# Optimization experiments

Hardware: AMD Instinct MI355X
Metric: run time of the kernel (lower is better)

## Reference

```python
import jax, jax.numpy as jnp
import numpy as np

N = 512      # nodes
E = 512      # edges = nb-graph nodes
M = 16384    # nb-graph edges
FIN = 64     # in_node_nf
HID = 128    # hidden_nf
D = 32       # VTV_coord_nf (positional-encoding width)


def _silu(v):
    return v * jax.nn.sigmoid(v)


def _mlp(v, w1, b1, w2, b2):
    # 2-layer MLP with SiLU (matches MLP(in, out, [hidden]))
    return _silu(v @ w1 + b1) @ w2 + b2


def setup_inputs() -> dict:
    key = jax.random.key(0)
    ks = jax.random.split(key, 32)

    def lin(k, i, o, scale=None):
        s = (1.0 / np.sqrt(i)) if scale is None else scale
        return jax.random.normal(k, (i, o), dtype=jnp.float32) * jnp.float32(s)

    inp = {}
    inp['h'] = jax.random.normal(ks[0], (N, FIN), dtype=jnp.float32)
    inp['x'] = jax.random.normal(ks[1], (N, 3), dtype=jnp.float32)
    inp['edges'] = jax.random.randint(ks[2], (2, E), 0, N)
    inp['nb_edge'] = jax.random.randint(ks[3], (2, M), 0, E)
    inp['edge_attr'] = jax.random.normal(ks[4], (E, 4), dtype=jnp.float32)
    inp['nb_num_nodes'] = E  # python int (static)
    # edge_encoder: MLP(2*FIN -> HID -> FIN)
    inp['ew1'] = lin(ks[5], 2 * FIN, HID); inp['eb1'] = jnp.zeros((HID,), jnp.float32)
    inp['ew2'] = lin(ks[6], HID, FIN);     inp['eb2'] = jnp.zeros((FIN,), jnp.float32)
    # PPGN mlp1 / mlp2: MLP(D+FIN -> HID -> FIN)
    inp['p1w1'] = lin(ks[7], D + FIN, HID); inp['p1b1'] = jnp.zeros((HID,), jnp.float32)
    inp['p1w2'] = lin(ks[8], HID, FIN);     inp['p1b2'] = jnp.zeros((FIN,), jnp.float32)
    inp['p2w1'] = lin(ks[9], D + FIN, HID); inp['p2b1'] = jnp.zeros((HID,), jnp.float32)
    inp['p2w2'] = lin(ks[10], HID, FIN);    inp['p2b2'] = jnp.zeros((FIN,), jnp.float32)
    # PPGN output mlp: MLP(D+FIN+FIN -> HID -> FIN) on concat(skip, matmul)
    inp['p3w1'] = lin(ks[11], D + 2 * FIN, HID); inp['p3b1'] = jnp.zeros((HID,), jnp.float32)
    inp['p3w2'] = lin(ks[12], HID, FIN);         inp['p3b2'] = jnp.zeros((FIN,), jnp.float32)
    # IGN 2->1: linear over 5 basis ops
    inp['ign_w'] = lin(ks[13], 5 * FIN, FIN); inp['ign_b'] = jnp.zeros((FIN,), jnp.float32)
    # coord_mlp: Linear(FIN,HID), SiLU, Linear(HID,1,bias=False) with tiny init
    inp['cw1'] = lin(ks[14], FIN, HID); inp['cb1'] = jnp.zeros((HID,), jnp.float32)
    inp['cw2'] = lin(ks[15], HID, 1, scale=0.001)
    # node_dec: MLP(FIN -> HID -> FIN)
    inp['ndw1'] = lin(ks[16], FIN, HID); inp['ndb1'] = jnp.zeros((HID,), jnp.float32)
    inp['ndw2'] = lin(ks[17], HID, FIN); inp['ndb2'] = jnp.zeros((FIN,), jnp.float32)
    return inp


def reference(h, x, edges, nb_edge, edge_attr, nb_num_nodes,
              ew1, eb1, ew2, eb2,
              p1w1, p1b1, p1w2, p1b2,
              p2w1, p2b1, p2w2, p2b2,
              p3w1, p3b1, p3w2, p3b2,
              ign_w, ign_b,
              cw1, cb1, cw2,
              ndw1, ndb1, ndw2, ndb2):
    rows, cols = edges[0], edges[1]
    coord_diff = x[rows] - x[cols]                      # [E,3]
    nbr, nbc = nb_edge[0], nb_edge[1]
    # VTV: inner product of the two relative-position vectors of paired edges
    vtv = jnp.sum(coord_diff[nbr] * coord_diff[nbc], axis=-1)   # [M]
    # sinusoidal positional encoding, a_scale = D/2
    half = D // 2
    div_term = jnp.exp(jnp.log(jnp.float32(10000.0)) * (2.0 * jnp.arange(half, dtype=jnp.float32) / D))
    ang = vtv[:, None] * jnp.float32(D / 2) / div_term          # [M, D/2]
    pe = jnp.stack([jnp.sin(ang), jnp.cos(ang)], axis=-1).reshape(vtv.shape[0], D)
    # node-pair features per original edge
    efn = _mlp(jnp.concatenate([h[rows], h[cols]], axis=1), ew1, eb1, ew2, eb2)  # [E,FIN]
    nb_feat = jnp.concatenate([pe, efn[nbr] * efn[nbc]], axis=1)                 # [M, D+FIN]
    # densify nb-graph 2-tensor and run PPGN block
    En = nb_num_nodes
    T = jnp.zeros((En, En, nb_feat.shape[1]), dtype=nb_feat.dtype).at[nbr, nbc].add(nb_feat)
    m1 = _mlp(T, p1w1, p1b1, p1w2, p1b2)                 # [En,En,FIN]
    m2 = _mlp(T, p2w1, p2b1, p2w2, p2b2)
    mult = jnp.einsum('ikf,kjf->ijf', m1, m2)            # feature-wise matmul
    Tout = _mlp(jnp.concatenate([T, mult], axis=-1), p3w1, p3b1, p3w2, p3b2)
    # IGN 2->1: diag, row-sum, col-sum, total-sum, trace (broadcast)
    idx = jnp.arange(En)
    diag = Tout[idx, idx]                                # [En,FIN]
    rowsum = Tout.sum(axis=1)
    colsum = Tout.sum(axis=0)
    tot = jnp.broadcast_to(Tout.sum(axis=(0, 1)), diag.shape)
    tr = jnp.broadcast_to(diag.sum(axis=0), diag.shape)
    nb_t1 = jnp.concatenate([diag, rowsum, colsum, tot, tr], axis=1) @ ign_w + ign_b  # [En,FIN]
    # coord update: weighted coord_diff, segment-mean over source node
    w = _silu(nb_t1 @ cw1 + cb1) @ cw2                   # [E,1]
    trans = coord_diff * w
    Nn = x.shape[0]
    seg = jax.ops.segment_sum(trans, rows, num_segments=Nn)
    cnt = jax.ops.segment_sum(jnp.ones((rows.shape[0], 1), trans.dtype), rows, num_segments=Nn)
    x_new = x + seg / jnp.clip(cnt, 1.0)
    # node update: scatter_add edge features then residual MLP
    nb_t0 = jax.ops.segment_sum(nb_t1, rows, num_segments=Nn)
    h_new = h + _mlp(nb_t0, ndw1, ndb1, ndw2, ndb2)
    return (h_new, x_new, edge_attr)
```

## Files before the change

### kernel.cpp

```cpp
#include <hip/hip_runtime.h>
#include <hip/hip_bf16.h>

#define NN   512
#define EE   512
#define MM   16384

typedef float v4f __attribute__((ext_vector_type(4)));
typedef short short8v __attribute__((ext_vector_type(8)));

__device__ __forceinline__ float silu_f(float v) { return v / (1.0f + __expf(-v)); }

__global__ __launch_bounds__(128) void k_edge(
    const float* __restrict__ h, const float* __restrict__ x,
    const int* __restrict__ edges,
    const float* __restrict__ ew1, const float* __restrict__ eb1,
    const float* __restrict__ ew2, const float* __restrict__ eb2,
    float* __restrict__ coord_diff, float* __restrict__ efn) {
  __shared__ float hin[128];
  __shared__ float hs[128];
  int e = blockIdx.x;
  int t = threadIdx.x;
  int r = edges[e], c = edges[EE + e];
  if (t < 3) coord_diff[e * 3 + t] = x[r * 3 + t] - x[c * 3 + t];
  if (t < 64) { hin[t] = h[r * 64 + t]; hin[64 + t] = h[c * 64 + t]; }
  __syncthreads();
  float acc = eb1[t];
  for (int k = 0; k < 128; ++k) acc += hin[k] * ew1[k * 128 + t];
  hs[t] = silu_f(acc);
  __syncthreads();
  if (t < 64) {
    float o = eb2[t];
    for (int k = 0; k < 128; ++k) o += hs[k] * ew2[k * 64 + t];
    efn[e * 64 + t] = o;
  }
}

__global__ __launch_bounds__(128) void k_consts(
    const float* __restrict__ p1b1, const float* __restrict__ p1w2, const float* __restrict__ p1b2,
    const float* __restrict__ p2b1, const float* __restrict__ p2w2, const float* __restrict__ p2b2,
    float* __restrict__ c1, float* __restrict__ c2) {
  __shared__ float h1[128], h2[128];
  int t = threadIdx.x;
  h1[t] = silu_f(p1b1[t]); h2[t] = silu_f(p2b1[t]);
  __syncthreads();
  if (t < 64) {
    float a1 = p1b2[t], a2 = p2b2[t];
    for (int k = 0; k < 128; ++k) { a1 += h1[k] * p1w2[k * 64 + t]; a2 += h2[k] * p2w2[k * 64 + t]; }
    c1[t] = a1; c2[t] = a2;
  }
}

__global__ __launch_bounds__(256) void k_prep(const float* __restrict__ p3w1,
                                              __hip_bfloat16* __restrict__ Wt) {
  int e = blockIdx.x * 256 + threadIdx.x;
  int hh = e >> 6, f = e & 63;
  Wt[hh * 64 + f] = __float2bfloat16(p3w1[(96 + f) * 128 + hh]);
}

__global__ __launch_bounds__(256) void k_mark(const int* __restrict__ nb_edge,
                                              int* __restrict__ slotmap) {
  int m = blockIdx.x * 256 + threadIdx.x;
  if (m >= MM) return;
  int cell = nb_edge[m] * 512 + nb_edge[MM + m];
  atomicCAS(&slotmap[cell], -1, -2);
}

__global__ __launch_bounds__(256) void k_compact(int* __restrict__ slotmap,
                                                 int* __restrict__ slotmapT,
                                                 int* __restrict__ cells,
                                                 int* __restrict__ nC) {
  int cell = blockIdx.x * 256 + threadIdx.x;
  if (slotmap[cell] != -2) return;
  int s = atomicAdd(nC, 1);
  slotmap[cell] = s;
  slotmapT[(cell & 511) * 512 + (cell >> 9)] = s;
  cells[s] = cell;
}

__global__ __launch_bounds__(192) void k_scatterT(
    const int* __restrict__ nb_edge, const int* __restrict__ slotmap,
    const float* __restrict__ coord_diff, const float* __restrict__ efn,
    float* __restrict__ Tc) {
  int t = threadIdx.x;
  int sub = (t >= 96) ? 1 : 0;
  int c = t - sub * 96;
  int m = blockIdx.x * 2 + sub;
  int a = nb_edge[m], b = nb_edge[MM + m];
  int s = slotmap[a * 512 + b];
  float val;
  if (c < 32) {
    float vtv = coord_diff[a * 3 + 0] * coord_diff[b * 3 + 0]
              + coord_diff[a * 3 + 1] * coord_diff[b * 3 + 1]
              + coord_diff[a * 3 + 2] * coord_diff[b * 3 + 2];
    int i = c >> 1;
    float ang = vtv * 16.0f * __expf(-0.57564627324851143f * (float)i);
    val = (c & 1) ? cosf(ang) : sinf(ang);
  } else {
    int f = c - 32;
    val = efn[a * 64 + f] * efn[b * 64 + f];
  }
  atomicAdd(&Tc[s * 96 + c], val);
}

__global__ __launch_bounds__(128) void k_mlp96b(
    const int* __restrict__ cells, const int* __restrict__ nC, const float* __restrict__ Tc,
    const float* __restrict__ w11, const float* __restrict__ b11,
    const float* __restrict__ w12, const float* __restrict__ b12,
    const float* __restrict__ w21, const float* __restrict__ b21,
    const float* __restrict__ w22, const float* __restrict__ b22,
    const float* __restrict__ c1, const float* __restrict__ c2,
    const float* __restrict__ p3w1,
    float* __restrict__ D1, float* __restrict__ D2,
    float* __restrict__ A, float* __restrict__ B,
    float* __restrict__ TWc) {
  __shared__ float xsT[96 * 8];
  __shared__ float hid[8][128];
  __shared__ int cl[8];
  int t = threadIdx.x;
  int nc = *nC;
  int s0 = blockIdx.x * 8;
  if (s0 >= nc) return;
  for (int e = t; e < 768; e += 128) xsT[(e % 96) * 8 + e / 96] = Tc[s0 * 96 + e];
  if (t < 8) cl[t] = (s0 + t < nc) ? cells[s0 + t] : 0;
  __syncthreads();
  float tw[8], a1[8], a2[8];
#pragma unroll
  for (int c = 0; c < 8; ++c) { tw[c] = 0.f; a1[c] = b11[t]; a2[c] = b21[t]; }
  for (int k = 0; k < 96; ++k) {
    float wt = p3w1[k * 128 + t];
    float w1v = w11[k * 128 + t];
    float w2v = w21[k * 128 + t];
    float4 xlo = *(const float4*)&xsT[k * 8];
    float4 xhi = *(const float4*)&xsT[k * 8 + 4];
    float xv[8] = {xlo.x, xlo.y, xlo.z, xlo.w, xhi.x, xhi.y, xhi.z, xhi.w};
#pragma unroll
    for (int c = 0; c < 8; ++c) {
      tw[c] += xv[c] * wt; a1[c] += xv[c] * w1v; a2[c] += xv[c] * w2v;
    }
  }
#pragma unroll
  for (int c = 0; c < 8; ++c) {
    if (s0 + c < nc) TWc[(s0 + c) * 128 + t] = tw[c];
    hid[c][t] = silu_f(a1[c]);
  }
  __syncthreads();
  {
    int hh = t & 63, cq = t >> 6;
    float o[4];
#pragma unroll
    for (int cc = 0; cc < 4; ++cc) o[cc] = b12[hh];
    for (int k = 0; k < 128; ++k) {
      float w = w12[k * 64 + hh];
#pragma unroll
      for (int cc = 0; cc < 4; ++cc) o[cc] += hid[cq * 4 + cc][k] * w;
    }
#pragma unroll
    for (int cc = 0; cc < 4; ++cc) {
      int c = cq * 4 + cc;
      if (s0 + c < nc) {
        float d = o[cc] - c1[hh];
        D1[(s0 + c) * 64 + hh] = d;
        atomicAdd(&A[(cl[c] >> 9) * 64 + hh], d);
      }
    }
  }
  __syncthreads();
#pragma unroll
  for (int c = 0; c < 8; ++c) hid[c][t] = silu_f(a2[c]);
  __syncthreads();
  {
    int hh = t & 63, cq = t >> 6;
    float o[4];
#pragma unroll
    for (int cc = 0; cc < 4; ++cc) o[cc] = b22[hh];
    for (int k = 0; k < 128; ++k) {
      float w = w22[k * 64 + hh];
#pragma unroll
      for (int cc = 0; cc < 4; ++cc) o[cc] += hid[cq * 4 + cc][k] * w;
    }
#pragma unroll
    for (int cc = 0; cc < 4; ++cc) {
      int c = cq * 4 + cc;
      if (s0 + c < nc) {
        float d = o[cc] - c2[hh];
        D2[(s0 + c) * 64 + hh] = d;
        atomicAdd(&B[(cl[c] & 511) * 64 + hh], d);
      }
    }
  }
}

__global__ __launch_bounds__(128) void k_uv(
    const float* __restrict__ A, const float* __restrict__ B,
    const float* __restrict__ c1, const float* __restrict__ c2,
    const float* __restrict__ p3w1, const float* __restrict__ p3b1,
    float* __restrict__ u, float* __restrict__ v) {
  __shared__ float vec[64];
  int i = blockIdx.x, y = blockIdx.y, t = threadIdx.x;
  if (t < 64)
    vec[t] = (y == 0) ? (512.0f * c1[t] * c2[t] + c2[t] * A[i * 64 + t])
                      : (c1[t] * B[i * 64 + t]);
  __syncthreads();
  float a = (y == 0) ? p3b1[t] : 0.f;
  for (int f = 0; f < 64; ++f) a += vec[f] * p3w1[(96 + f) * 128 + t];
  (y == 0 ? u : v)[i * 128 + t] = a;
}

__global__ __launch_bounds__(512) void k_densify(
    const int* __restrict__ slotmap, const int* __restrict__ slotmapT,
    const float* __restrict__ D1, const float* __restrict__ D2,
    __hip_bfloat16* __restrict__ D1d, __hip_bfloat16* __restrict__ D2dT) {
  int k = threadIdx.x;
  int i = blockIdx.x;
  int y = blockIdx.y;
  if (y < 64) {
    int f = y;
    int s = slotmap[i * 512 + k];
    float v = (s >= 0) ? D1[s * 64 + f] : 0.f;
    D1d[(f * 512 + i) * 512 + k] = __float2bfloat16(v);
  } else {
    int f = y - 64;
    int s = slotmapT[i * 512 + k];
    float v = (s >= 0) ? D2[s * 64 + f] : 0.f;
    D2dT[(f * 512 + i) * 512 + k] = __float2bfloat16(v);
  }
}

__global__ __launch_bounds__(256) void k_einsum_mfma(
    const __hip_bfloat16* __restrict__ D1d,
    const __hip_bfloat16* __restrict__ D2dT,
    __hip_bfloat16* __restrict__ S_fij) {
  __shared__ short As[128 * 40];
  __shared__ short Bs[128 * 40];
  int b = blockIdx.x;
  int f = b >> 4;
  int i0 = ((b >> 2) & 3) * 128, j0 = (b & 3) * 128;
  int t = threadIdx.x;
  int w = t >> 6, lane = t & 63;
  int wy = w >> 1, wx = w & 1;
  int q = lane >> 4, l15 = lane & 15;
  const short* Ap = (const short*)D1d + f * 262144;
  const short* Bp = (const short*)D2dT + f * 262144;
  int row = t >> 1, seg = t & 1;
  v4f acc[4][4];
#pragma unroll
  for (int yi = 0; yi < 4; ++yi)
#pragma unroll
    for (int xj = 0; xj < 4; ++xj) acc[yi][xj] = (v4f){0.f, 0.f, 0.f, 0.f};
  for (int k0 = 0; k0 < 512; k0 += 32) {
    __syncthreads();
    const short8v* ga = (const short8v*)&Ap[(i0 + row) * 512 + k0 + seg * 16];
    const short8v* gb = (const short8v*)&Bp[(j0 + row) * 512 + k0 + seg * 16];
    *(short8v*)&As[row * 40 + seg * 16] = ga[0];
    *(short8v*)&As[row * 40 + seg * 16 + 8] = ga[1];
    *(short8v*)&Bs[row * 40 + seg * 16] = gb[0];
    *(short8v*)&Bs[row * 40 + seg * 16 + 8] = gb[1];
    __syncthreads();
    short8v af[4], bf[4];
#pragma unroll
    for (int x = 0; x < 4; ++x) {
      af[x] = *(const short8v*)&As[(wy * 64 + x * 16 + l15) * 40 + q * 8];
      bf[x] = *(const short8v*)&Bs[(wx * 64 + x * 16 + l15) * 40 + q * 8];
    }
#pragma unroll
    for (int yi = 0; yi < 4; ++yi)
#pragma unroll
      for (int xj = 0; xj < 4; ++xj)
        acc[yi][xj] = __builtin_amdgcn_mfma_f32_16x16x32_bf16(af[yi], bf[xj], acc[yi][xj], 0, 0, 0);
  }
#pragma unroll
  for (int yi = 0; yi < 4; ++yi)
#pragma unroll
    for (int r = 0; r < 4; ++r) {
      int irow = i0 + wy * 64 + yi * 16 + q * 4 + r;
#pragma unroll
      for (int xj = 0; xj < 4; ++xj)
        S_fij[(f * 512 + irow) * 512 + j0 + wx * 64 + xj * 16 + l15] =
            __float2bfloat16(acc[yi][xj][r]);
    }
}

__global__ __launch_bounds__(256) void k_transpose(
    const __hip_bfloat16* __restrict__ S_fij, __hip_bfloat16* __restrict__ S) {
  __shared__ short lds[64 * 72];
  int t = threadIdx.x;
  int ij0 = blockIdx.x * 64;
  const short* src = (const short*)S_fij;
#pragma unroll
  for (int p = 0; p < 2; ++p) {
    int f = p * 32 + (t >> 3), seg = t & 7;
    short8v ga = *(const short8v*)&src[f * 262144 + ij0 + seg * 8];
    int fgrp = f >> 3, flo = f & 7;
#pragma unroll
    for (int k = 0; k < 8; ++k) {
      int ij = seg * 8 + k;
      int swz = (fgrp ^ (ij & 7) ^ ((ij >> 3) & 7)) & 7;
      lds[ij * 72 + swz * 8 + flo] = ga[k];
    }
  }
  __syncthreads();
  short* dst = (short*)S;
#pragma unroll
  for (int p = 0; p < 2; ++p) {
    int ij = p * 32 + (t >> 3), fseg = t & 7;
    int swz = (fseg ^ (ij & 7) ^ ((ij >> 3) & 7)) & 7;
    short8v val = *(const short8v*)&lds[ij * 72 + swz * 8];
    *(short8v*)&dst[(ij0 + ij) * 64 + fseg * 8] = val;
  }
}

__global__ __launch_bounds__(256) void k_tout_mfma(
    const __hip_bfloat16* __restrict__ S, const float* __restrict__ u,
    const float* __restrict__ v, const float* __restrict__ TWc,
    const int* __restrict__ slotmap, const __hip_bfloat16* __restrict__ Wt,
    float* __restrict__ row_part, float* __restrict__ col_part,
    float* __restrict__ diag_silu) {
  __shared__ __hip_bfloat16 WtL[128 * 72];
  __shared__ float uvL[4096];
  __shared__ float colbuf[4][16][128];
  __shared__ int slotL[256];
  int t = threadIdx.x;
  int w = t >> 6, lane = t & 63;
  int q = lane >> 4, l15 = lane & 15;
  int bi = blockIdx.x >> 5, bj = blockIdx.x & 31;
  int i0 = bi * 16, j0 = bj * 16;
  for (int e = t; e < 4096; e += 256) {
    int row = e >> 5, c2 = e & 31;
    ((unsigned*)WtL)[row * 36 + c2] = ((const unsigned*)Wt)[row * 32 + c2];
  }
  for (int e = t; e < 2048; e += 256) uvL[e] = u[(i0 + (e >> 7)) * 128 + (e & 127)];
  for (int e = t; e < 2048; e += 256) uvL[2048 + e] = v[(j0 + (e >> 7)) * 128 + (e & 127)];
  slotL[t] = slotmap[(i0 + (t >> 4)) * 512 + j0 + (t & 15)];
  short8v a[4][2];
#pragma unroll
  for (int mt = 0; mt < 4; ++mt) {
    const short8v* sp =
        (const short8v*)&S[((i0 + w * 4 + mt) * 512 + j0 + l15) * 64];
    a[mt][0] = sp[q];
    a[mt][1] = sp[4 + q];
  }
  __syncthreads();
#pragma unroll
  for (int half = 0; half < 2; ++half) {
    v4f acc[4][4];
#pragma unroll
    for (int mt = 0; mt < 4; ++mt)
#pragma unroll
      for (int n4 = 0; n4 < 4; ++n4) {
        int nt = half * 4 + n4;
        const short8v* b0 = (const short8v*)&WtL[(nt * 16 + l15) * 72 + q * 8];
        const short8v* b1 = (const short8v*)&WtL[(nt * 16 + l15) * 72 + 32 + q * 8];
        v4f c = {0.f, 0.f, 0.f, 0.f};
        c = __builtin_amdgcn_mfma_f32_16x16x32_bf16(a[mt][0], *b0, c, 0, 0, 0);
        c = __builtin_amdgcn_mfma_f32_16x16x32_bf16(a[mt][1], *b1, c, 0, 0, 0);
        acc[mt][n4] = c;
      }
#pragma unroll
    for (int n4 = 0; n4 < 4; ++n4) {
      int nt = half * 4 + n4;
      int hh = nt * 16 + l15;
      float rs[4] = {0.f, 0.f, 0.f, 0.f};
#pragma unroll
      for (int r = 0; r < 4; ++r) {
        int jL = q * 4 + r;
        float cs = 0.f;
        float vv = uvL[2048 + jL * 128 + hh];
#pragma unroll
        for (int mt = 0; mt < 4; ++mt) {
          int iL = w * 4 + mt;
          float z = acc[mt][n4][r] + uvL[iL * 128 + hh] + vv;
          int s = slotL[iL * 16 + jL];
          if (s >= 0) z += TWc[s * 128 + hh];
          float sv = silu_f(z);
          rs[mt] += sv;
          cs += sv;
          if (bi == bj && iL == jL) diag_silu[(i0 + iL) * 128 + hh] = sv;
        }
        colbuf[w][jL][hh] = cs;
      }
#pragma unroll
      for (int mt = 0; mt < 4; ++mt) {
        float rsum = rs[mt];
        rsum += __shfl_xor(rsum, 16);
        rsum += __shfl_xor(rsum, 32);
        if (q == 0)
          row_part[(bj * 512 + i0 + w * 4 + mt) * 128 + hh] = rsum;
      }
    }
  }
  __syncthreads();
  for (int e = t; e < 2048; e += 256) {
    int jL = e >> 7, hh = e & 127;
    float acc4 = colbuf[0][jL][hh] + colbuf[1][jL][hh] +
                 colbuf[2][jL][hh] + colbuf[3][jL][hh];
    col_part[(bi * 512 + j0 + jL) * 128 + hh] = acc4;
  }
}

__global__ __launch_bounds__(256) void k_sumparts(
    const float* __restrict__ row_part, const float* __restrict__ col_part,
    float* __restrict__ rowsum, float* __restrict__ colsum) {
  int i = blockIdx.x, t = threadIdx.x;
  const float* src = (t < 128) ? row_part : col_part;
  float* dst = (t < 128) ? rowsum : colsum;
  int hc = t & 127;
  float a = 0.f;
  for (int p = 0; p < 32; ++p) a += src[(p * 512 + i) * 128 + hc];
  dst[i * 128 + hc] = a;
}

__global__ __launch_bounds__(64) void k_tout2(
    const float* __restrict__ diag_silu, const float* __restrict__ rowsum_silu,
    const float* __restrict__ colsum_silu,
    const float* __restrict__ w2, const float* __restrict__ b2,
    float* __restrict__ diag_T, float* __restrict__ row_T, float* __restrict__ col_T) {
  __shared__ float in[128];
  int e = blockIdx.x, which = blockIdx.y, t = threadIdx.x;
  const float* src = (which == 0) ? diag_silu : (which == 1) ? rowsum_silu : colsum_silu;
  in[t] = src[e * 128 + t]; in[64 + t] = src[e * 128 + 64 + t];
  __syncthreads();
  float a = 0.f;
  for (int k = 0; k < 128; ++k) a += in[k] * w2[k * 64 + t];
  float bias = b2[t] * ((which == 0) ? 1.0f : 512.0f);
  float* dst = (which == 0) ? diag_T : (which == 1) ? row_T : col_T;
  dst[e * 64 + t] = a + bias;
}

__global__ __launch_bounds__(128) void k_totr(
    const float* __restrict__ row_T, const float* __restrict__ diag_T,
    float* __restrict__ tot, float* __restrict__ tr) {
  int t = threadIdx.x;
  const float* src = (t < 64) ? row_T : diag_T;
  int f = t & 63;
  float a = 0.f;
  for (int e = 0; e < 512; ++e) a += src[e * 64 + f];
  if (t < 64) tot[f] = a; else tr[f] = a;
}

__global__ __launch_bounds__(64) void k_nbt1(
    const float* __restrict__ diag_T, const float* __restrict__ row_T,
    const float* __restrict__ col_T, const float* __restrict__ tot,
    const float* __restrict__ tr,
    const float* __restrict__ gw, const float* __restrict__ gb,
    float* __restrict__ nb_t1) {
  __shared__ float in[320];
  int e = blockIdx.x, t = threadIdx.x;
  in[t] = diag_T[e * 64 + t]; in[64 + t] = row_T[e * 64 + t];
  in[128 + t] = col_T[e * 64 + t]; in[192 + t] = tot[t]; in[256 + t] = tr[t];
  __syncthreads();
  float a = gb[t];
  for (int k = 0; k < 320; ++k) a += in[k] * gw[k * 64 + t];
  nb_t1[e * 64 + t] = a;
}

__global__ __launch_bounds__(128) void k_edge_out(
    const int* __restrict__ edges, const float* __restrict__ coord_diff,
    const float* __restrict__ nb_t1, const float* __restrict__ edge_attr,
    const float* __restrict__ cw1, const float* __restrict__ cb1,
    const float* __restrict__ cw2,
    float* __restrict__ seg, float* __restrict__ cnt, float* __restrict__ nb_t0,
    float* __restrict__ out_ea) {
  __shared__ float in[64];
  __shared__ float red[128];
  int e = blockIdx.x, t = threadIdx.x;
  if (t < 64) in[t] = nb_t1[e * 64 + t];
  __syncthreads();
  float a = cb1[t];
  for (int k = 0; k < 64; ++k) a += in[k] * cw1[k * 128 + t];
  red[t] = silu_f(a) * cw2[t];
  __syncthreads();
  for (int s2 = 64; s2 > 0; s2 >>= 1) {
    if (t < s2) red[t] += red[t + s2];
    __syncthreads();
  }
  float w = red[0];
  int r = edges[e];
  if (t < 3) atomicAdd(&seg[r * 3 + t], coord_diff[e * 3 + t] * w);
  if (t == 64) atomicAdd(&cnt[r], 1.0f);
  if (t < 64) atomicAdd(&nb_t0[r * 64 + t], in[t]);
  if (t < 4) out_ea[e * 4 + t] = edge_attr[e * 4 + t];
}

__global__ __launch_bounds__(128) void k_node_out(
    const float* __restrict__ h, const float* __restrict__ x,
    const float* __restrict__ seg, const float* __restrict__ cnt,
    const float* __restrict__ nb_t0,
    const float* __restrict__ w1, const float* __restrict__ b1,
    const float* __restrict__ w2, const float* __restrict__ b2,
    float* __restrict__ out_h, float* __restrict__ out_x) {
  __shared__ float in[64];
  __shared__ float hs[128];
  int n = blockIdx.x, t = threadIdx.x;
  if (t < 3) {
    float c = cnt[n]; if (c < 1.f) c = 1.f;
    out_x[n * 3 + t] = x[n * 3 + t] + seg[n * 3 + t] / c;
  }
  if (t < 64) in[t] = nb_t0[n * 64 + t];
  __syncthreads();
  float a = b1[t];
  for (int k = 0; k < 64; ++k) a += in[k] * w1[k * 128 + t];
  hs[t] = silu_f(a);
  __syncthreads();
  if (t < 64) {
    float o = b2[t];
    for (int k = 0; k < 128; ++k) o += hs[k] * w2[k * 64 + t];
    out_h[n * 64 + t] = h[n * 64 + t] + o;
  }
}

extern "C" void kernel_launch(void* const* d_in, const int* in_sizes, int n_in,
                              void* d_out, int out_size, void* d_ws, size_t ws_size,
                              hipStream_t stream) {
  (void)in_sizes; (void)n_in; (void)out_size; (void)ws_size;
  const float* h  = (const float*)d_in[0];
  const float* x  = (const float*)d_in[1];
  const int* edges   = (const int*)d_in[2];
  const int* nb_edge = (const int*)d_in[3];
  const float* edge_attr = (const float*)d_in[4];
  const float* ew1 = (const float*)d_in[6],  *eb1 = (const float*)d_in[7];
  const float* ew2 = (const float*)d_in[8],  *eb2 = (const float*)d_in[9];
  const float* p1w1 = (const float*)d_in[10], *p1b1 = (const float*)d_in[11];
  const float* p1w2 = (const float*)d_in[12], *p1b2 = (const float*)d_in[13];
  const float* p2w1 = (const float*)d_in[14], *p2b1 = (const float*)d_in[15];
  const float* p2w2 = (const float*)d_in[16], *p2b2 = (const float*)d_in[17];
  const float* p3w1 = (const float*)d_in[18], *p3b1 = (const float*)d_in[19];
  const float* p3w2 = (const float*)d_in[20], *p3b2 = (const float*)d_in[21];
  const float* ignw = (const float*)d_in[22], *ignb = (const float*)d_in[23];
  const float* cw1 = (const float*)d_in[24], *cb1 = (const float*)d_in[25];
  const float* cw2 = (const float*)d_in[26];
  const float* ndw1 = (const float*)d_in[27], *ndb1 = (const float*)d_in[28];
  const float* ndw2 = (const float*)d_in[29], *ndb2 = (const float*)d_in[30];

  char* ws = (char*)d_ws;
  __hip_bfloat16* D1d  = (__hip_bfloat16*)(ws + 0);
  __hip_bfloat16* S    = (__hip_bfloat16*)(ws + 0);
  __hip_bfloat16* D2dT = (__hip_bfloat16*)(ws + 33554432);
  __hip_bfloat16* S_fij = (__hip_bfloat16*)(ws + 67108864);
  float* row_part = (float*)(ws + 100663296);
  float* col_part = (float*)(ws + 117440512);
  float* Tc    = (float*)(ws + 134217728);
  int*   nC    = (int*)(ws + 140509184);
  float* A     = (float*)(ws + 140509200);
  float* B     = (float*)(ws + 140640272);
  float* seg   = (float*)(ws + 140771344);
  float* cnt   = (float*)(ws + 140777488);
  float* nb_t0 = (float*)(ws + 140779536);
  int*   slotmap  = (int*)(ws + 140910608);
  int*   slotmapT = (int*)(ws + 141959184);
  int*   cells    = (int*)(ws + 143007760);
  float* D1       = (float*)(ws + 143073296);
  float* D2       = (float*)(ws + 147267600);
  float* TWc      = (float*)(ws + 151461904);
  float* c1       = (float*)(ws + 159850512);
  float* c2       = (float*)(ws + 159850768);
  float* u        = (float*)(ws + 159851024);
  float* v        = (float*)(ws + 160113168);
  float* coord_diff  = (float*)(ws + 160375312);
  float* efn         = (float*)(ws + 160381456);
  float* diag_silu   = (float*)(ws + 160512528);
  float* rowsum_silu = (float*)(ws + 160774672);
  float* colsum_silu = (float*)(ws + 161036816);
  float* diag_T      = (float*)(ws + 161298960);
  float* row_T       = (float*)(ws + 161430032);
  float* col_T       = (float*)(ws + 161561104);
  float* tot         = (float*)(ws + 161692176);
  float* tr          = (float*)(ws + 161692432);
  float* nb_t1       = (float*)(ws + 161692688);
  __hip_bfloat16* Wt = (__hip_bfloat16*)(ws + 161823760);

  float* out_h  = (float*)d_out;
  float* out_x  = out_h + 512 * 64;
  float* out_ea = out_x + 512 * 3;

  hipMemsetAsync(slotmap, 0xFF, 2097152, stream);
  hipMemsetAsync(ws + 134217728, 0, 6692880, stream);

  k_edge<<<512, 128, 0, stream>>>(h, x, edges, ew1, eb1, ew2, eb2, coord_diff, efn);
  k_consts<<<1, 128, 0, stream>>>(p1b1, p1w2, p1b2, p2b1, p2w2, p2b2, c1, c2);
  k_prep<<<32, 256, 0, stream>>>(p3w1, Wt);
  k_mark<<<64, 256, 0, stream>>>(nb_edge, slotmap);
  k_compact<<<1024, 256, 0, stream>>>(slotmap, slotmapT, cells, nC);
  k_scatterT<<<8192, 192, 0, stream>>>(nb_edge, slotmap, coord_diff, efn, Tc);
  k_mlp96b<<<2048, 128, 0, stream>>>(cells, nC, Tc,
                                     p1w1, p1b1, p1w2, p1b2,
                                     p2w1, p2b1, p2w2, p2b2,
                                     c1, c2, p3w1, D1, D2, A, B, TWc);
  k_uv<<<dim3(512, 2), 128, 0, stream>>>(A, B, c1, c2, p3w1, p3b1, u, v);
  k_densify<<<dim3(512, 128), 512, 0, stream>>>(slotmap, slotmapT, D1, D2, D1d, D2dT);
  k_einsum_mfma<<<1024, 256, 0, stream>>>(D1d, D2dT, S_fij);
  k_transpose<<<4096, 256, 0, stream>>>(S_fij, S);
  k_tout_mfma<<<1024, 256, 0, stream>>>(S, u, v, TWc, slotmap, Wt,
                                        row_part, col_part, diag_silu);
  k_sumparts<<<512, 256, 0, stream>>>(row_part, col_part, rowsum_silu, colsum_silu);
  k_tout2<<<dim3(512, 3), 64, 0, stream>>>(diag_silu, rowsum_silu, colsum_silu,
                                           p3w2, p3b2, diag_T, row_T, col_T);
  k_totr<<<1, 128, 0, stream>>>(row_T, diag_T, tot, tr);
  k_nbt1<<<512, 64, 0, stream>>>(diag_T, row_T, col_T, tot, tr, ignw, ignb, nb_t1);
  k_edge_out<<<512, 128, 0, stream>>>(edges, coord_diff, nb_t1, edge_attr,
                                      cw1, cb1, cw2, seg, cnt, nb_t0, out_ea);
  k_node_out<<<512, 128, 0, stream>>>(h, x, seg, cnt, nb_t0,
                                      ndw1, ndb1, ndw2, ndb2, out_h, out_x);
}
```

Before: 443.3 us.

## Use bf16 weights in sparse MLP, double cells per block, shrink tout LDS

Adds a prep kernel that converts the PPGN MLP weights to bf16. k_mlp96b now reads those bf16 weights and handles 16 cells per block instead of 8, halving its grid, so weight traffic per cell drops and each loaded weight is reused more. In k_tout_mfma the u/v staging and column-partial buffers are stored in LDS as bf16 to cut shared-memory footprint, which may raise occupancy. The cost is lower precision in weights and column partial sums, more registers per thread in the MLP kernel, and one extra launch.

After: 460.3 us. 1.04x slower.

```diff
diff --git a/kernel.cpp b/kernel.cpp
--- a/kernel.cpp
+++ b/kernel.cpp
@@ -55,6 +55,21 @@
   int e = blockIdx.x * 256 + threadIdx.x;
   int hh = e >> 6, f = e & 63;
   Wt[hh * 64 + f] = __float2bfloat16(p3w1[(96 + f) * 128 + hh]);
+}
+
+__global__ __launch_bounds__(256) void k_prepw(
+    const float* __restrict__ w11, const float* __restrict__ w21,
+    const float* __restrict__ p3w1,
+    const float* __restrict__ w12, const float* __restrict__ w22,
+    __hip_bfloat16* __restrict__ w11b, __hip_bfloat16* __restrict__ w21b,
+    __hip_bfloat16* __restrict__ pw1b,
+    __hip_bfloat16* __restrict__ w12b, __hip_bfloat16* __restrict__ w22b) {
+  int e = blockIdx.x * 256 + threadIdx.x;
+  if (e < 12288) w11b[e] = __float2bfloat16(w11[e]);
+  else if (e < 24576) w21b[e - 12288] = __float2bfloat16(w21[e - 12288]);
+  else if (e < 36864) pw1b[e - 24576] = __float2bfloat16(p3w1[e - 24576]);
+  else if (e < 45056) w12b[e - 36864] = __float2bfloat16(w12[e - 36864]);
+  else if (e < 53248) w22b[e - 45056] = __float2bfloat16(w22[e - 45056]);
 }
 
 __global__ __launch_bounds__(256) void k_mark(const int* __restrict__ nb_edge,
@@ -104,59 +119,62 @@
 
 __global__ __launch_bounds__(128) void k_mlp96b(
     const int* __restrict__ cells, const int* __restrict__ nC, const float* __restrict__ Tc,
-    const float* __restrict__ w11, const float* __restrict__ b11,
-    const float* __restrict__ w12, const float* __restrict__ b12,
-    const float* __restrict__ w21, const float* __restrict__ b21,
-    const float* __restrict__ w22, const float* __restrict__ b22,
+    const __hip_bfloat16* __restrict__ w11b, const float* __restrict__ b11,
+    const __hip_bfloat16* __restrict__ w12b, const float* __restrict__ b12,
+    const __hip_bfloat16* __restrict__ w21b, const float* __restrict__ b21,
+    const __hip_bfloat16* __restrict__ w22b, const float* __restrict__ b22,
     const float* __restrict__ c1, const float* __restrict__ c2,
-    const float* __restrict__ p3w1,
+    const __hip_bfloat16* __restrict__ pw1b,
     float* __restrict__ D1, float* __restrict__ D2,
     float* __restrict__ A, float* __restrict__ B,
     float* __restrict__ TWc) {
-  __shared__ float xsT[96 * 8];
-  __shared__ float hid[8][128];
-  __shared__ int cl[8];
+  __shared__ float xsT[96 * 16];
+  __shared__ float hid[16][128];
+  __shared__ int cl[16];
   int t = threadIdx.x;
   int nc = *nC;
-  int s0 = blockIdx.x * 8;
+  int s0 = blockIdx.x * 16;
   if (s0 >= nc) return;
-  for (int e = t; e < 768; e += 128) xsT[(e % 96) * 8 + e / 96] = Tc[s0 * 96 + e];
-  if (t < 8) cl[t] = (s0 + t < nc) ? cells[s0 + t] : 0;
-  __syncthreads();
-  float tw[8], a1[8], a2[8];
-#pragma unroll
-  for (int c = 0; c < 8; ++c) { tw[c] = 0.f; a1[c] = b11[t]; a2[c] = b21[t]; }
+  for (int e = t; e < 1536; e += 128) xsT[(e % 96) * 16 + e / 96] = Tc[s0 * 96 + e];
+  if (t < 16) cl[t] = (s0 + t < nc) ? cells[s0 + t] : 0;
+  __syncthreads();
+  float tw[16], a1[16], a2[16];
+#pragma unroll
+  for (int c = 0; c < 16; ++c) { tw[c] = 0.f; a1[c] = b11[t]; a2[c] = b21[t]; }
   for (int k = 0; k < 96; ++k) {
-    float wt = p3w1[k * 128 + t];
-    float w1v = w11[k * 128 + t];
-    float w2v = w21[k * 128 + t];
-    float4 xlo = *(const float4*)&xsT[k * 8];
-    float4 xhi = *(const float4*)&xsT[k * 8 + 4];
-    float xv[8] = {xlo.x, xlo.y, xlo.z, xlo.w, xhi.x, xhi.y, xhi.z, xhi.w};
-#pragma unroll
-    for (int c = 0; c < 8; ++c) {
+    float wt = __bfloat162float(pw1b[k * 128 + t]);
+    float w1v = __bfloat162float(w11b[k * 128 + t]);
+    float w2v = __bfloat162float(w21b[k * 128 + t]);
+    float4 x0 = *(const float4*)&xsT[k * 16];
+    float4 x1 = *(const float4*)&xsT[k * 16 + 4];
+    float4 x2 = *(const float4*)&xsT[k * 16 + 8];
+    float4 x3 = *(const float4*)&xsT[k * 16 + 12];
+    float xv[16] = {x0.x, x0.y, x0.z, x0.w, x1.x, x1.y, x1.z, x1.w,
+                    x2.x, x2.y, x2.z, x2.w, x3.x, x3.y, x3.z, x3.w};
+#pragma unroll
+    for (int c = 0; c < 16; ++c) {
       tw[c] += xv[c] * wt; a1[c] += xv[c] * w1v; a2[c] += xv[c] * w2v;
     }
   }
 #pragma unroll
-  for (int c = 0; c < 8; ++c) {
+  for (int c = 0; c < 16; ++c) {
     if (s0 + c < nc) TWc[(s0 + c) * 128 + t] = tw[c];
     hid[c][t] = silu_f(a1[c]);
   }
   __syncthreads();
   {
     int hh = t & 63, cq = t >> 6;
-    float o[4];
-#pragma unroll
-    for (int cc = 0; cc < 4; ++cc) o[cc] = b12[hh];
+    float o[8];
+#pragma unroll
+    for (int cc = 0; cc < 8; ++cc) o[cc] = b12[hh];
     for (int k = 0; k < 128; ++k) {
-      float w = w12[k * 64 + hh];
-#pragma unroll
-      for (int cc = 0; cc < 4; ++cc) o[cc] += hid[cq * 4 + cc][k] * w;
-    }
-#pragma unroll
-    for (int cc = 0; cc < 4; ++cc) {
-      int c = cq * 4 + cc;
+      float w = __bfloat162float(w12b[k * 64 + hh]);
+#pragma unroll
+      for (int cc = 0; cc < 8; ++cc) o[cc] += hid[cq * 8 + cc][k] * w;
+    }
+#pragma unroll
+    for (int cc = 0; cc < 8; ++cc) {
+      int c = cq * 8 + cc;
       if (s0 + c < nc) {
         float d = o[cc] - c1[hh];
         D1[(s0 + c) * 64 + hh] = d;
@@ -166,21 +184,21 @@
   }
   __syncthreads();
 #pragma unroll
-  for (int c = 0; c < 8; ++c) hid[c][t] = silu_f(a2[c]);
+  for (int c = 0; c < 16; ++c) hid[c][t] = silu_f(a2[c]);
   __syncthreads();
   {
     int hh = t & 63, cq = t >> 6;
-    float o[4];
-#pragma unroll
-    for (int cc = 0; cc < 4; ++cc) o[cc] = b22[hh];
+    float o[8];
+#pragma unroll
+    for (int cc = 0; cc < 8; ++cc) o[cc] = b22[hh];
     for (int k = 0; k < 128; ++k) {
-      float w = w22[k * 64 + hh];
-#pragma unroll
-      for (int cc = 0; cc < 4; ++cc) o[cc] += hid[cq * 4 + cc][k] * w;
-    }
-#pragma unroll
-    for (int cc = 0; cc < 4; ++cc) {
-      int c = cq * 4 + cc;
+      float w = __bfloat162float(w22b[k * 64 + hh]);
+#pragma unroll
+      for (int cc = 0; cc < 8; ++cc) o[cc] += hid[cq * 8 + cc][k] * w;
+    }
+#pragma unroll
+    for (int cc = 0; cc < 8; ++cc) {
+      int c = cq * 8 + cc;
       if (s0 + c < nc) {
         float d = o[cc] - c2[hh];
         D2[(s0 + c) * 64 + hh] = d;
@@ -316,8 +334,8 @@
     float* __restrict__ row_part, float* __restrict__ col_part,
     float* __restrict__ diag_silu) {
   __shared__ __hip_bfloat16 WtL[128 * 72];
-  __shared__ float uvL[4096];
-  __shared__ float colbuf[4][16][128];
+  __shared__ __hip_bfloat16 uvL[4096];
+  __shared__ __hip_bfloat16 colbuf[4][16][140];
   __shared__ int slotL[256];
   int t = threadIdx.x;
   int w = t >> 6, lane = t & 63;
@@ -328,8 +346,10 @@
     int row = e >> 5, c2 = e & 31;
     ((unsigned*)WtL)[row * 36 + c2] = ((const unsigned*)Wt)[row * 32 + c2];
   }
-  for (int e = t; e < 2048; e += 256) uvL[e] = u[(i0 + (e >> 7)) * 128 + (e & 127)];
-  for (int e = t; e < 2048; e += 256) uvL[2048 + e] = v[(j0 + (e >> 7)) * 128 + (e & 127)];
+  for (int e = t; e < 2048; e += 256)
+    uvL[e] = __float2bfloat16(u[(i0 + (e >> 7)) * 128 + (e & 127)]);
+  for (int e = t; e < 2048; e += 256)
+    uvL[2048 + e] = __float2bfloat16(v[(j0 + (e >> 7)) * 128 + (e & 127)]);
   slotL[t] = slotmap[(i0 + (t >> 4)) * 512 + j0 + (t & 15)];
   short8v a[4][2];
 #pragma unroll
@@ -364,11 +384,11 @@
       for (int r = 0; r < 4; ++r) {
         int jL = q * 4 + r;
         float cs = 0.f;
-        float vv = uvL[2048 + jL * 128 + hh];
+        float vv = __bfloat162float(uvL[2048 + jL * 128 + hh]);
 #pragma unroll
         for (int mt = 0; mt < 4; ++mt) {
           int iL = w * 4 + mt;
-          float z = acc[mt][n4][r] + uvL[iL * 128 + hh] + vv;
+          float z = acc[mt][n4][r] + __bfloat162float(uvL[iL * 128 + hh]) + vv;
           int s = slotL[iL * 16 + jL];
           if (s >= 0) z += TWc[s * 128 + hh];
           float sv = silu_f(z);
@@ -376,7 +396,7 @@
           cs += sv;
           if (bi == bj && iL == jL) diag_silu[(i0 + iL) * 128 + hh] = sv;
         }
-        colbuf[w][jL][hh] = cs;
+        colbuf[w][jL][hh] = __float2bfloat16(cs);
       }
 #pragma unroll
       for (int mt = 0; mt < 4; ++mt) {
@@ -391,8 +411,8 @@
   __syncthreads();
   for (int e = t; e < 2048; e += 256) {
     int jL = e >> 7, hh = e & 127;
-    float acc4 = colbuf[0][jL][hh] + colbuf[1][jL][hh] +
-                 colbuf[2][jL][hh] + colbuf[3][jL][hh];
+    float acc4 = __bfloat162float(colbuf[0][jL][hh]) + __bfloat162float(colbuf[1][jL][hh]) +
+                 __bfloat162float(colbuf[2][jL][hh]) + __bfloat162float(colbuf[3][jL][hh]);
     col_part[(bi * 512 + j0 + jL) * 128 + hh] = acc4;
   }
 }
@@ -567,6 +587,11 @@
   float* tr          = (float*)(ws + 161692432);
   float* nb_t1       = (float*)(ws + 161692688);
   __hip_bfloat16* Wt = (__hip_bfloat16*)(ws + 161823760);
+  __hip_bfloat16* w11b = (__hip_bfloat16*)(ws + 161840144);
+  __hip_bfloat16* w21b = (__hip_bfloat16*)(ws + 161864720);
+  __hip_bfloat16* pw1b = (__hip_bfloat16*)(ws + 161889296);
+  __hip_bfloat16* w12b = (__hip_bfloat16*)(ws + 161913872);
+  __hip_bfloat16* w22b = (__hip_bfloat16*)(ws + 161930256);
 
   float* out_h  = (float*)d_out;
   float* out_x  = out_h + 512 * 64;
@@ -578,13 +603,15 @@
   k_edge<<<512, 128, 0, stream>>>(h, x, edges, ew1, eb1, ew2, eb2, coord_diff, efn);
   k_consts<<<1, 128, 0, stream>>>(p1b1, p1w2, p1b2, p2b1, p2w2, p2b2, c1, c2);
   k_prep<<<32, 256, 0, stream>>>(p3w1, Wt);
+  k_prepw<<<208, 256, 0, stream>>>(p1w1, p2w1, p3w1, p1w2, p2w2,
+                                   w11b, w21b, pw1b, w12b, w22b);
   k_mark<<<64, 256, 0, stream>>>(nb_edge, slotmap);
   k_compact<<<1024, 256, 0, stream>>>(slotmap, slotmapT, cells, nC);
   k_scatterT<<<8192, 192, 0, stream>>>(nb_edge, slotmap, coord_diff, efn, Tc);
-  k_mlp96b<<<2048, 128, 0, stream>>>(cells, nC, Tc,
-                                     p1w1, p1b1, p1w2, p1b2,
-                                     p2w1, p2b1, p2w2, p2b2,
-                                     c1, c2, p3w1, D1, D2, A, B, TWc);
+  k_mlp96b<<<1024, 128, 0, stream>>>(cells, nC, Tc,
+                                     w11b, p1b1, w12b, p1b2,
+                                     w21b, p2b1, w22b, p2b2,
+                                     c1, c2, pw1b, D1, D2, A, B, TWc);
   k_uv<<<dim3(512, 2), 128, 0, stream>>>(A, B, c1, c2, p3w1, p3b1, u, v);
   k_densify<<<dim3(512, 128), 512, 0, stream>>>(slotmap, slotmapT, D1, D2, D1d, D2dT);
   k_einsum_mfma<<<1024, 256, 0, stream>>>(D1d, D2dT, S_fij);
```

## Pre-transpose D1/D2 to feature-major bf16 and shrink tout LDS buffers to bf16

Applied to the files above, without the earlier changes.

Adds a kernel that transposes the sparse D1/D2 value arrays into a feature-major bf16 layout. The densify gather then reads 2-byte values from a per-feature contiguous array instead of strided fp32 rows, cutting the footprint of the random gathers. Separately, k_tout_mfma now keeps u/v and its column-partial buffers in LDS as bf16 to reduce shared memory use and raise occupancy. This adds precision loss on u, v and the column partial sums, plus one extra launch.

Measured after the change: 456.8 us. 3.0% more time.

```diff
diff --git a/kernel.cpp b/kernel.cpp
--- a/kernel.cpp
+++ b/kernel.cpp
@@ -206,24 +206,42 @@
   (y == 0 ? u : v)[i * 128 + t] = a;
 }
 
+__global__ __launch_bounds__(256) void k_dtrans(
+    const float* __restrict__ D1, const float* __restrict__ D2,
+    __hip_bfloat16* __restrict__ D1T, __hip_bfloat16* __restrict__ D2T) {
+  __shared__ float tile[64][65];
+  int t = threadIdx.x;
+  int s0 = blockIdx.x * 64;
+  const float* src = blockIdx.y ? D2 : D1;
+  __hip_bfloat16* dst = blockIdx.y ? D2T : D1T;
+#pragma unroll 4
+  for (int p = 0; p < 16; ++p) {
+    int row = p * 4 + (t >> 6), f = t & 63;
+    tile[row][f] = src[(s0 + row) * 64 + f];
+  }
+  __syncthreads();
+#pragma unroll 4
+  for (int p = 0; p < 16; ++p) {
+    int f = p * 4 + (t >> 6), so = t & 63;
+    dst[f * 16384 + s0 + so] = __float2bfloat16(tile[so][f]);
+  }
+}
+
 __global__ __launch_bounds__(512) void k_densify(
     const int* __restrict__ slotmap, const int* __restrict__ slotmapT,
-    const float* __restrict__ D1, const float* __restrict__ D2,
+    const __hip_bfloat16* __restrict__ D1T, const __hip_bfloat16* __restrict__ D2T,
     __hip_bfloat16* __restrict__ D1d, __hip_bfloat16* __restrict__ D2dT) {
   int k = threadIdx.x;
   int i = blockIdx.x;
   int y = blockIdx.y;
-  if (y < 64) {
-    int f = y;
-    int s = slotmap[i * 512 + k];
-    float v = (s >= 0) ? D1[s * 64 + f] : 0.f;
-    D1d[(f * 512 + i) * 512 + k] = __float2bfloat16(v);
-  } else {
-    int f = y - 64;
-    int s = slotmapT[i * 512 + k];
-    float v = (s >= 0) ? D2[s * 64 + f] : 0.f;
-    D2dT[(f * 512 + i) * 512 + k] = __float2bfloat16(v);
-  }
+  const int* sm = (y < 64) ? slotmap : slotmapT;
+  const unsigned short* srcT =
+      (const unsigned short*)((y < 64) ? D1T : D2T);
+  unsigned short* dst = (unsigned short*)((y < 64) ? D1d : D2dT);
+  int f = y & 63;
+  int s = sm[i * 512 + k];
+  unsigned short v = (s >= 0) ? srcT[f * 16384 + s] : (unsigned short)0;
+  dst[(f * 512 + i) * 512 + k] = v;
 }
 
 __global__ __launch_bounds__(256) void k_einsum_mfma(
@@ -316,8 +334,8 @@
     float* __restrict__ row_part, float* __restrict__ col_part,
     float* __restrict__ diag_silu) {
   __shared__ __hip_bfloat16 WtL[128 * 72];
-  __shared__ float uvL[4096];
-  __shared__ float colbuf[4][16][128];
+  __shared__ __hip_bfloat16 uvL[4096];
+  __shared__ __hip_bfloat16 colbuf[4][16][140];
   __shared__ int slotL[256];
   int t = threadIdx.x;
   int w = t >> 6, lane = t & 63;
@@ -328,8 +346,10 @@
     int row = e >> 5, c2 = e & 31;
     ((unsigned*)WtL)[row * 36 + c2] = ((const unsigned*)Wt)[row * 32 + c2];
   }
-  for (int e = t; e < 2048; e += 256) uvL[e] = u[(i0 + (e >> 7)) * 128 + (e & 127)];
-  for (int e = t; e < 2048; e += 256) uvL[2048 + e] = v[(j0 + (e >> 7)) * 128 + (e & 127)];
+  for (int e = t; e < 2048; e += 256)
+    uvL[e] = __float2bfloat16(u[(i0 + (e >> 7)) * 128 + (e & 127)]);
+  for (int e = t; e < 2048; e += 256)
+    uvL[2048 + e] = __float2bfloat16(v[(j0 + (e >> 7)) * 128 + (e & 127)]);
   slotL[t] = slotmap[(i0 + (t >> 4)) * 512 + j0 + (t & 15)];
   short8v a[4][2];
 #pragma unroll
@@ -364,11 +384,11 @@
       for (int r = 0; r < 4; ++r) {
         int jL = q * 4 + r;
         float cs = 0.f;
-        float vv = uvL[2048 + jL * 128 + hh];
+        float vv = __bfloat162float(uvL[2048 + jL * 128 + hh]);
 #pragma unroll
         for (int mt = 0; mt < 4; ++mt) {
           int iL = w * 4 + mt;
-          float z = acc[mt][n4][r] + uvL[iL * 128 + hh] + vv;
+          float z = acc[mt][n4][r] + __bfloat162float(uvL[iL * 128 + hh]) + vv;
           int s = slotL[iL * 16 + jL];
           if (s >= 0) z += TWc[s * 128 + hh];
           float sv = silu_f(z);
@@ -376,7 +396,7 @@
           cs += sv;
           if (bi == bj && iL == jL) diag_silu[(i0 + iL) * 128 + hh] = sv;
         }
-        colbuf[w][jL][hh] = cs;
+        colbuf[w][jL][hh] = __float2bfloat16(cs);
       }
 #pragma unroll
       for (int mt = 0; mt < 4; ++mt) {
@@ -391,8 +411,8 @@
   __syncthreads();
   for (int e = t; e < 2048; e += 256) {
     int jL = e >> 7, hh = e & 127;
-    float acc4 = colbuf[0][jL][hh] + colbuf[1][jL][hh] +
-                 colbuf[2][jL][hh] + colbuf[3][jL][hh];
+    float acc4 = __bfloat162float(colbuf[0][jL][hh]) + __bfloat162float(colbuf[1][jL][hh]) +
+                 __bfloat162float(colbuf[2][jL][hh]) + __bfloat162float(colbuf[3][jL][hh]);
     col_part[(bi * 512 + j0 + jL) * 128 + hh] = acc4;
   }
 }
@@ -566,7 +586,9 @@
   float* tot         = (float*)(ws + 161692176);
   float* tr          = (float*)(ws + 161692432);
   float* nb_t1       = (float*)(ws + 161692688);
-  __hip_bfloat16* Wt = (__hip_bfloat16*)(ws + 161823760);
+  __hip_bfloat16* Wt  = (__hip_bfloat16*)(ws + 161823760);
+  __hip_bfloat16* D1T = (__hip_bfloat16*)(ws + 161840144);
+  __hip_bfloat16* D2T = (__hip_bfloat16*)(ws + 163937296);
 
   float* out_h  = (float*)d_out;
   float* out_x  = out_h + 512 * 64;
@@ -586,7 +608,8 @@
                                      p2w1, p2b1, p2w2, p2b2,
                                      c1, c2, p3w1, D1, D2, A, B, TWc);
   k_uv<<<dim3(512, 2), 128, 0, stream>>>(A, B, c1, c2, p3w1, p3b1, u, v);
-  k_densify<<<dim3(512, 128), 512, 0, stream>>>(slotmap, slotmapT, D1, D2, D1d, D2dT);
+  k_dtrans<<<dim3(256, 2), 256, 0, stream>>>(D1, D2, D1T, D2T);
+  k_densify<<<dim3(512, 128), 512, 0, stream>>>(slotmap, slotmapT, D1T, D2T, D1d, D2dT);
   k_einsum_mfma<<<1024, 256, 0, stream>>>(D1d, D2dT, S_fij);
   k_transpose<<<4096, 256, 0, stream>>>(S_fij, S);
   k_tout_mfma<<<1024, 256, 0, stream>>>(S, u, v, TWc, slotmap, Wt,
```
